# Kernel tuning notes

Measured on AMD Instinct MI355X. Metric: run time of the kernel, lower is better.

Reference implementation:

```python
import jax, jax.numpy as jnp
import numpy as np

D_MODEL = 768
N_HEADS = 12
NUM_EXPERTS = 4
TOP_K = 2
SPAN_LEN = 64
GATE_HIDDEN = 128


def setup_inputs() -> dict:
    key = jax.random.key(0)
    ks = jax.random.split(key, 14)
    B, T, C, E = 4, 4096, D_MODEL, NUM_EXPERTS
    s = 0.02
    return {
        "hidden_states": jax.random.normal(ks[0], (B, T, C), jnp.float32),
        "Wq": jax.random.normal(ks[1], (E, C, C), jnp.float32) * s,
        "bq": jnp.zeros((E, C), jnp.float32),
        "Wk": jax.random.normal(ks[2], (E, C, C), jnp.float32) * s,
        "bk": jnp.zeros((E, C), jnp.float32),
        "Wv": jax.random.normal(ks[3], (E, C, C), jnp.float32) * s,
        "bv": jnp.zeros((E, C), jnp.float32),
        "gW1": jax.random.normal(ks[4], (GATE_HIDDEN, C), jnp.float32) * s,
        "gb1": jnp.zeros((GATE_HIDDEN,), jnp.float32),
        "gW2": jax.random.normal(ks[5], (E, GATE_HIDDEN), jnp.float32) * s,
        "gb2": jnp.zeros((E,), jnp.float32),
        "Wo": jax.random.normal(ks[6], (C, C), jnp.float32) * s,
        "bo": jnp.zeros((C,), jnp.float32),
    }


def _moe_proj(w, x, W, b):
    # per-expert projection then gate-weighted sum over experts
    # x: (B,N,S,C), W: (E,O,C), w: (B,N,E)
    proj = jnp.einsum("bnsc,eoc->ebnso", x, W)          # (E,B,N,S,C)
    out = jnp.einsum("bne,ebnso->bnso", w, proj)
    out = out + jnp.einsum("bne,eo->bno", w, b)[:, :, None, :]
    return out


def reference(hidden_states, Wq, bq, Wk, bk, Wv, bv, gW1, gb1, gW2, gb2, Wo, bo):
    B, T, C = hidden_states.shape
    S, H, E, K = SPAN_LEN, N_HEADS, NUM_EXPERTS, TOP_K
    Dh = C // H
    N = T // S  # T is a multiple of span_len -> no padding, all-ones masks
    x = hidden_states.reshape(B, N, S, C)

    # gating: mean-pool per span -> MLP -> top-k softmax scattered to E slots
    pooled = x.mean(axis=2)                                  # (B,N,C)
    h = jax.nn.relu(pooled @ gW1.T + gb1)
    logits = h @ gW2.T + gb2                                 # (B,N,E)
    vals, idx = jax.lax.top_k(logits, K)
    sm = jax.nn.softmax(vals, axis=-1)                       # (B,N,K)
    w = jnp.sum(jax.nn.one_hot(idx, E, dtype=sm.dtype) * sm[..., None], axis=-2)  # (B,N,E)
    entropy = -jnp.mean(jnp.sum(w * jnp.log(jnp.clip(w, 1e-9)), axis=-1))

    # gate-weighted expert QKV projections
    q = _moe_proj(w, x, Wq, bq).reshape(B, N, S, H, Dh)
    k = _moe_proj(w, x, Wk, bk).reshape(B, N, S, H, Dh)
    v = _moe_proj(w, x, Wv, bv).reshape(B, N, S, H, Dh)

    # per-span attention (mask is all ones; dropout in eval mode)
    scores = jnp.einsum("bnshd,bnthd->bnhst", q, k) / jnp.sqrt(jnp.float32(Dh))
    attn = jax.nn.softmax(scores, axis=-1)
    out = jnp.einsum("bnhst,bnthd->bnshd", attn, v).reshape(B, T, C)
    out = out @ Wo.T + bo
    return out, entropy
```

## Files before the change

### kernel.cpp

```cpp
#include <hip/hip_runtime.h>
#include <hip/hip_bf16.h>
#include <hip/hip_fp16.h>

typedef _Float16 f16;
typedef _Float16 f16x8 __attribute__((ext_vector_type(8)));
typedef _Float16 f16x4 __attribute__((ext_vector_type(4)));
typedef float f32x4 __attribute__((ext_vector_type(4)));

constexpr int B = 4;
constexpr int T = 4096;
constexpr int C = 768;
constexpr int NH = 12;
constexpr int DH = 64;
constexpr int E = 4;
constexpr int SPAN = 64;
constexpr int N = T / SPAN;
constexpr int BN = B * N;
constexpr int GH = 128;
constexpr int BTC = B * T * C;

constexpr int U_WE = E * C * C / 8;
constexpr int U_WO = C * C / 8;
constexpr int U_WTOT = 3 * U_WE + U_WO;

__global__ __launch_bounds__(768) void cvt_x_pool(
    const float* __restrict__ x, f16* __restrict__ x16,
    float* __restrict__ pooled) {
    int span = blockIdx.x;
    int tid = threadIdx.x;
    int u = tid % 96, rg = tid / 96;
    __shared__ float part[8][C];

    const float* xb = x + (size_t)span * SPAN * C;
    f16* xo = x16 + (size_t)span * SPAN * C;
    float a8[8] = {};
    #pragma unroll
    for (int j = 0; j < 8; ++j) {
        int r = rg * 8 + j;
        const float4* s = (const float4*)(xb + (size_t)r * C + u * 8);
        float4 A = s[0], Bv = s[1];
        f16x8 o;
        o[0] = (f16)A.x;  o[1] = (f16)A.y;  o[2] = (f16)A.z;  o[3] = (f16)A.w;
        o[4] = (f16)Bv.x; o[5] = (f16)Bv.y; o[6] = (f16)Bv.z; o[7] = (f16)Bv.w;
        *(f16x8*)(xo + (size_t)r * C + u * 8) = o;
        a8[0] += A.x;  a8[1] += A.y;  a8[2] += A.z;  a8[3] += A.w;
        a8[4] += Bv.x; a8[5] += Bv.y; a8[6] += Bv.z; a8[7] += Bv.w;
    }
    #pragma unroll
    for (int j = 0; j < 8; ++j) part[rg][u * 8 + j] = a8[j];
    __syncthreads();
    float s = 0.f;
    #pragma unroll
    for (int g = 0; g < 8; ++g) s += part[g][tid];
    pooled[(size_t)span * C + tid] = s * (1.f / 64.f);
}

__global__ void cvt_w(const float* __restrict__ Wq, const float* __restrict__ Wk,
                      const float* __restrict__ Wv, const float* __restrict__ Wo,
                      f16* __restrict__ Wq16, f16* __restrict__ Wk16,
                      f16* __restrict__ Wv16, f16* __restrict__ Wo16) {
    int i = blockIdx.x * blockDim.x + threadIdx.x;
    int stride = gridDim.x * blockDim.x;
    for (; i < U_WTOT; i += stride) {
        const float* src; f16* dst; int u;
        if (i < U_WE)               { src = Wq; dst = Wq16; u = i; }
        else if (i < 2 * U_WE)      { src = Wk; dst = Wk16; u = i - U_WE; }
        else if (i < 3 * U_WE)      { src = Wv; dst = Wv16; u = i - 2 * U_WE; }
        else                        { src = Wo; dst = Wo16; u = i - 3 * U_WE; }
        float4 a = ((const float4*)src)[2 * u];
        float4 b = ((const float4*)src)[2 * u + 1];
        f16x8 o;
        o[0] = (f16)a.x; o[1] = (f16)a.y; o[2] = (f16)a.z; o[3] = (f16)a.w;
        o[4] = (f16)b.x; o[5] = (f16)b.y; o[6] = (f16)b.z; o[7] = (f16)b.w;
        ((f16x8*)dst)[u] = o;
    }
}

__global__ __launch_bounds__(128) void gate_mlp(
    const float* __restrict__ pooled,
    const float* __restrict__ gW1, const float* __restrict__ gb1,
    const float* __restrict__ gW2, const float* __restrict__ gb2,
    int* __restrict__ eidx, float* __restrict__ ewts,
    float* __restrict__ ent_partial) {
    int span = blockIdx.x;
    int tid = threadIdx.x;
    __shared__ float pl[C];
    __shared__ float h[GH];
    __shared__ float logits[E];

    for (int c = tid; c < C; c += 128) pl[c] = pooled[(size_t)span * C + c];
    __syncthreads();

    {
        float acc = gb1[tid];
        const float* wrow = gW1 + (size_t)tid * C;
        #pragma unroll 8
        for (int c = 0; c < C; ++c) acc += pl[c] * wrow[c];
        h[tid] = acc > 0.f ? acc : 0.f;
    }
    __syncthreads();

    if (tid < E) {
        float acc = gb2[tid];
        const float* wrow = gW2 + (size_t)tid * GH;
        #pragma unroll 8
        for (int j = 0; j < GH; ++j) acc += h[j] * wrow[j];
        logits[tid] = acc;
    }
    __syncthreads();

    if (tid == 0) {
        int i0 = 0; float v0 = logits[0];
        for (int e = 1; e < E; ++e) { if (logits[e] > v0) { v0 = logits[e]; i0 = e; } }
        int i1 = -1; float v1 = -3.0e38f;
        for (int e = 0; e < E; ++e) { if (e != i0 && logits[e] > v1) { v1 = logits[e]; i1 = e; } }
        float bq_ = expf(v1 - v0);
        float s = 1.f + bq_;
        float sm0 = 1.f / s;
        float sm1 = bq_ / s;
        eidx[span * 2 + 0] = i0;
        eidx[span * 2 + 1] = i1;
        ewts[span * 2 + 0] = sm0;
        ewts[span * 2 + 1] = sm1;
        float p0 = fmaxf(sm0, 1e-9f), p1 = fmaxf(sm1, 1e-9f);
        ent_partial[span] = sm0 * logf(p0) + sm1 * logf(p1);
    }
}

__global__ void entropy_kernel(const float* __restrict__ ent_partial, float* __restrict__ out_ent) {
    __shared__ float sh[256];
    int tid = threadIdx.x;
    sh[tid] = ent_partial[tid];
    __syncthreads();
    for (int s = 128; s > 0; s >>= 1) {
        if (tid < s) sh[tid] += sh[tid + s];
        __syncthreads();
    }
    if (tid == 0) *out_ent = -sh[0] * (1.0f / (float)BN);
}

__global__ __launch_bounds__(256) void qkv_mfma(
    const f16* __restrict__ xh,
    const f16* __restrict__ Wq16, const float* __restrict__ bq,
    const f16* __restrict__ Wk16, const float* __restrict__ bk,
    const f16* __restrict__ Wv16, const float* __restrict__ bv,
    const int* __restrict__ eidx, const float* __restrict__ ewts,
    f16* __restrict__ q16, f16* __restrict__ k16, f16* __restrict__ vt)
{
    int span  = blockIdx.x;
    int otile = blockIdx.y;
    int proj  = blockIdx.z;

    const f16* W; const float* bias; f16* out;
    if (proj == 0)      { W = Wq16; bias = bq; out = q16; }
    else if (proj == 1) { W = Wk16; bias = bk; out = k16; }
    else                { W = Wv16; bias = bv; out = vt; }

    int e0 = eidx[span * 2 + 0], e1 = eidx[span * 2 + 1];
    float w0 = ewts[span * 2 + 0], w1 = ewts[span * 2 + 1];
    f16 w0h = (f16)w0, w1h = (f16)w1;

    __shared__ f16x8 xs_u[64 * 8];
    __shared__ f16x8 ws_u[256 * 8];

    const f16x8* xu  = (const f16x8*)(xh + (size_t)span * 64 * C);
    const f16x8* Wu0 = (const f16x8*)(W + ((size_t)e0 * C + otile * 256) * (size_t)C);
    const f16x8* Wu1 = (const f16x8*)(W + ((size_t)e1 * C + otile * 256) * (size_t)C);

    int tid = threadIdx.x;
    int lane = tid & 63, wv = tid >> 6;
    int lr = lane & 15, lg = lane >> 4;

    f32x4 acc[4][4] = {};

    f16x8 xr[2], w0r[8], w1r[8];
    #pragma unroll
    for (int i = 0; i < 2; ++i) {
        int id = tid + i * 256;
        xr[i] = xu[(id >> 3) * 96 + (id & 7)];
    }
    #pragma unroll
    for (int i = 0; i < 8; ++i) {
        int id = tid + i * 256;
        w0r[i] = Wu0[(size_t)(id >> 3) * 96 + (id & 7)];
        w1r[i] = Wu1[(size_t)(id >> 3) * 96 + (id & 7)];
    }

    for (int kc8 = 0; kc8 < 96; kc8 += 8) {
        #pragma unroll
        for (int i = 0; i < 2; ++i) {
            int id = tid + i * 256;
            int r = id >> 3, u = id & 7;
            xs_u[r * 8 + (u ^ (r & 7))] = xr[i];
        }
        #pragma unroll
        for (int i = 0; i < 8; ++i) {
            int id = tid + i * 256;
            int r = id >> 3, u = id & 7;
            ws_u[r * 8 + (u ^ (r & 7))] = w0r[i] * w0h + w1r[i] * w1h;
        }

        if (kc8 < 88) {
            int kn = kc8 + 8;
            #pragma unroll
            for (int i = 0; i < 2; ++i) {
                int id = tid + i * 256;
                xr[i] = xu[(id >> 3) * 96 + kn + (id & 7)];
            }
            #pragma unroll
            for (int i = 0; i < 4; ++i) {
                int id = tid + i * 256;
                w0r[i] = Wu0[(size_t)(id >> 3) * 96 + kn + (id & 7)];
                w1r[i] = Wu1[(size_t)(id >> 3) * 96 + kn + (id & 7)];
            }
        }

        asm volatile("s_waitcnt lgkmcnt(0)" ::: "memory");
        __builtin_amdgcn_s_barrier();
        __builtin_amdgcn_sched_barrier(0);

        {
            int ub = lg;
            f16x8 afrag[4], bfrag[4];
            #pragma unroll
            for (int m = 0; m < 4; ++m) {
                int r = m * 16 + lr;
                afrag[m] = xs_u[r * 8 + (ub ^ (r & 7))];
            }
            #pragma unroll
            for (int n = 0; n < 4; ++n) {
                int r = wv * 64 + n * 16 + lr;
                bfrag[n] = ws_u[r * 8 + (ub ^ (r & 7))];
            }
            #pragma unroll
            for (int m = 0; m < 4; ++m)
                #pragma unroll
                for (int n = 0; n < 4; ++n)
                    acc[m][n] = __builtin_amdgcn_mfma_f32_16x16x32_f16(afrag[m], bfrag[n], acc[m][n], 0, 0, 0);
        }

        __builtin_amdgcn_sched_barrier(0);
        if (kc8 < 88) {
            int kn = kc8 + 8;
            #pragma unroll
            for (int i = 4; i < 8; ++i) {
                int id = tid + i * 256;
                w0r[i] = Wu0[(size_t)(id >> 3) * 96 + kn + (id & 7)];
                w1r[i] = Wu1[(size_t)(id >> 3) * 96 + kn + (id & 7)];
            }
        }
        __builtin_amdgcn_sched_barrier(0);

        {
            int ub = 4 + lg;
            f16x8 afrag[4], bfrag[4];
            #pragma unroll
            for (int m = 0; m < 4; ++m) {
                int r = m * 16 + lr;
                afrag[m] = xs_u[r * 8 + (ub ^ (r & 7))];
            }
            #pragma unroll
            for (int n = 0; n < 4; ++n) {
                int r = wv * 64 + n * 16 + lr;
                bfrag[n] = ws_u[r * 8 + (ub ^ (r & 7))];
            }
            #pragma unroll
            for (int m = 0; m < 4; ++m)
                #pragma unroll
                for (int n = 0; n < 4; ++n)
                    acc[m][n] = __builtin_amdgcn_mfma_f32_16x16x32_f16(afrag[m], bfrag[n], acc[m][n], 0, 0, 0);
        }

        asm volatile("s_waitcnt lgkmcnt(0)" ::: "memory");
        __builtin_amdgcn_s_barrier();
        __builtin_amdgcn_sched_barrier(0);
    }

    if (proj == 2) {
        f16* vtb = out + (size_t)span * C * 64;
        #pragma unroll
        for (int n = 0; n < 4; ++n) {
            int col = otile * 256 + wv * 64 + n * 16 + lr;
            float be = w0 * bias[(size_t)e0 * C + col] + w1 * bias[(size_t)e1 * C + col];
            #pragma unroll
            for (int m = 0; m < 4; ++m) {
                f16x4 pk;
                #pragma unroll
                for (int r = 0; r < 4; ++r) pk[r] = (f16)(acc[m][n][r] + be);
                *(f16x4*)&vtb[(size_t)col * 64 + m * 16 + lg * 4] = pk;
            }
        }
    } else {
        f16* outb = out + (size_t)span * 64 * C;
        #pragma unroll
        for (int n = 0; n < 4; ++n) {
            int col = otile * 256 + wv * 64 + n * 16 + lr;
            float be = w0 * bias[(size_t)e0 * C + col] + w1 * bias[(size_t)e1 * C + col];
            #pragma unroll
            for (int m = 0; m < 4; ++m) {
                #pragma unroll
                for (int r = 0; r < 4; ++r) {
                    int row = m * 16 + lg * 4 + r;
                    outb[(size_t)row * C + col] = (f16)(acc[m][n][r] + be);
                }
            }
        }
    }
}

__global__ __launch_bounds__(256) void attn_mfma(
    const f16* __restrict__ q16, const f16* __restrict__ k16,
    const f16* __restrict__ vt, f16* __restrict__ a16)
{
    int h = blockIdx.x, span = blockIdx.y;
    __shared__ __align__(16) f16 Klds[64 * 72];
    __shared__ __align__(16) f16 Vlds[64 * 72];
    __shared__ __align__(16) f16 Plds[64 * 72];

    int tid = threadIdx.x;
    int lane = tid & 63, mt = tid >> 6;
    int lr = lane & 15, lg = lane >> 4;

    const f16x8* ku = (const f16x8*)k16;
    const f16x8* vu = (const f16x8*)vt;
    #pragma unroll
    for (int i = 0; i < 2; ++i) {
        int id = tid + i * 256;
        int r = id >> 3, u = id & 7;
        *(f16x8*)&Klds[r * 72 + u * 8] = ku[(size_t)span * 6144 + (size_t)r * 96 + h * 8 + u];
        *(f16x8*)&Vlds[r * 72 + u * 8] = vu[(size_t)span * 6144 + (size_t)(h * 64 + r) * 8 + u];
    }
    __syncthreads();

    const f16x8* qu = (const f16x8*)q16;
    f16x8 qa[2];
    #pragma unroll
    for (int kk = 0; kk < 2; ++kk)
        qa[kk] = qu[(size_t)span * 6144 + (size_t)(mt * 16 + lr) * 96 + h * 8 + kk * 4 + lg];

    f32x4 accs[4] = {};
    #pragma unroll
    for (int nt = 0; nt < 4; ++nt) {
        #pragma unroll
        for (int kk = 0; kk < 2; ++kk) {
            f16x8 kb = *(const f16x8*)&Klds[(nt * 16 + lr) * 72 + kk * 32 + lg * 8];
            accs[nt] = __builtin_amdgcn_mfma_f32_16x16x32_f16(qa[kk], kb, accs[nt], 0, 0, 0);
        }
    }

    #pragma unroll
    for (int nt = 0; nt < 4; ++nt) accs[nt] *= 0.125f;
    f32x4 m4;
    #pragma unroll
    for (int r = 0; r < 4; ++r)
        m4[r] = fmaxf(fmaxf(accs[0][r], accs[1][r]), fmaxf(accs[2][r], accs[3][r]));
    #pragma unroll
    for (int st = 1; st < 16; st <<= 1) {
        #pragma unroll
        for (int r = 0; r < 4; ++r) m4[r] = fmaxf(m4[r], __shfl_xor(m4[r], st));
    }
    f32x4 ps[4];
    f32x4 sum4 = {0.f, 0.f, 0.f, 0.f};
    #pragma unroll
    for (int nt = 0; nt < 4; ++nt)
        #pragma unroll
        for (int r = 0; r < 4; ++r) {
            ps[nt][r] = __expf(accs[nt][r] - m4[r]);
            sum4[r] += ps[nt][r];
        }
    #pragma unroll
    for (int st = 1; st < 16; st <<= 1) {
        #pragma unroll
        for (int r = 0; r < 4; ++r) sum4[r] += __shfl_xor(sum4[r], st);
    }
    f32x4 inv4;
    #pragma unroll
    for (int r = 0; r < 4; ++r) inv4[r] = 1.0f / sum4[r];

    #pragma unroll
    for (int nt = 0; nt < 4; ++nt)
        #pragma unroll
        for (int r = 0; r < 4; ++r)
            Plds[(mt * 16 + lg * 4 + r) * 72 + nt * 16 + lr] = (f16)ps[nt][r];
    __syncthreads();

    f16x8 pa[2];
    #pragma unroll
    for (int kkt = 0; kkt < 2; ++kkt)
        pa[kkt] = *(const f16x8*)&Plds[(mt * 16 + lr) * 72 + kkt * 32 + lg * 8];
    f32x4 acco[4] = {};
    #pragma unroll
    for (int nt = 0; nt < 4; ++nt) {
        #pragma unroll
        for (int kkt = 0; kkt < 2; ++kkt) {
            f16x8 vb = *(const f16x8*)&Vlds[(nt * 16 + lr) * 72 + kkt * 32 + lg * 8];
            acco[nt] = __builtin_amdgcn_mfma_f32_16x16x32_f16(pa[kkt], vb, acco[nt], 0, 0, 0);
        }
    }

    #pragma unroll
    for (int nt = 0; nt < 4; ++nt)
        #pragma unroll
        for (int r = 0; r < 4; ++r)
            Klds[(mt * 16 + lg * 4 + r) * 72 + nt * 16 + lr] = (f16)(acco[nt][r] * inv4[r]);
    __syncthreads();

    int row = mt * 16 + (lane >> 2);
    int u2 = (lane & 3) * 2;
    f16x8 o0 = *(const f16x8*)&Klds[row * 72 + u2 * 8];
    f16x8 o1 = *(const f16x8*)&Klds[row * 72 + u2 * 8 + 8];
    f16x8* au = (f16x8*)a16;
    au[(size_t)span * 6144 + (size_t)row * 96 + h * 8 + u2]     = o0;
    au[(size_t)span * 6144 + (size_t)row * 96 + h * 8 + u2 + 1] = o1;
}

__global__ __launch_bounds__(512) void outproj_mfma(
    const f16* __restrict__ ah, const f16* __restrict__ Wo16,
    const float* __restrict__ bo, float* __restrict__ Y)
{
    int rt = blockIdx.x;
    int otile = blockIdx.y;

    __shared__ f16x8 as_u[128 * 8];
    __shared__ f16x8 ws_u[256 * 8];

    const f16x8* au  = (const f16x8*)(ah + (size_t)rt * 128 * C);
    const f16x8* Wou = (const f16x8*)(Wo16 + (size_t)otile * 256 * C);

    int tid = threadIdx.x;
    int lane = tid & 63, wv = tid >> 6;
    int lr = lane & 15, lg = lane >> 4;
    int wm = (wv >> 2) * 64;
    int wn = (wv & 3) * 64;

    f32x4 acc[4][4] = {};

    for (int kc8 = 0; kc8 < 96; kc8 += 8) {
        #pragma unroll
        for (int i = 0; i < 2; ++i) {
            int id = tid + i * 512;
            int r = id >> 3, u = id & 7;
            as_u[r * 8 + (u ^ (r & 7))] = au[(size_t)r * 96 + kc8 + u];
        }
        #pragma unroll
        for (int i = 0; i < 4; ++i) {
            int id = tid + i * 512;
            int r = id >> 3, u = id & 7;
            ws_u[r * 8 + (u ^ (r & 7))] = Wou[(size_t)r * 96 + kc8 + u];
        }
        __syncthreads();
        #pragma unroll
        for (int kk = 0; kk < 2; ++kk) {
            int ub = kk * 4 + lg;
            f16x8 afrag[4], bfrag[4];
            #pragma unroll
            for (int m = 0; m < 4; ++m) {
                int r = wm + m * 16 + lr;
                afrag[m] = as_u[r * 8 + (ub ^ (r & 7))];
            }
            #pragma unroll
            for (int n = 0; n < 4; ++n) {
                int r = wn + n * 16 + lr;
                bfrag[n] = ws_u[r * 8 + (ub ^ (r & 7))];
            }
            #pragma unroll
            for (int m = 0; m < 4; ++m)
                #pragma unroll
                for (int n = 0; n < 4; ++n)
                    acc[m][n] = __builtin_amdgcn_mfma_f32_16x16x32_f16(afrag[m], bfrag[n], acc[m][n], 0, 0, 0);
        }
        __syncthreads();
    }

    #pragma unroll
    for (int n = 0; n < 4; ++n) {
        int col = otile * 256 + wn + n * 16 + lr;
        float be = bo[col];
        #pragma unroll
        for (int m = 0; m < 4; ++m) {
            #pragma unroll
            for (int r = 0; r < 4; ++r) {
                int row = rt * 128 + wm + m * 16 + lg * 4 + r;
                Y[(size_t)row * C + col] = acc[m][n][r] + be;
            }
        }
    }
}

extern "C" void kernel_launch(void* const* d_in, const int* in_sizes, int n_in,
                              void* d_out, int out_size, void* d_ws, size_t ws_size,
                              hipStream_t stream) {
    const float* x   = (const float*)d_in[0];
    const float* Wq  = (const float*)d_in[1];
    const float* bq  = (const float*)d_in[2];
    const float* Wk  = (const float*)d_in[3];
    const float* bk  = (const float*)d_in[4];
    const float* Wv  = (const float*)d_in[5];
    const float* bv  = (const float*)d_in[6];
    const float* gW1 = (const float*)d_in[7];
    const float* gb1 = (const float*)d_in[8];
    const float* gW2 = (const float*)d_in[9];
    const float* gb2 = (const float*)d_in[10];
    const float* Wo  = (const float*)d_in[11];
    const float* bo  = (const float*)d_in[12];

    float* out = (float*)d_out;

    char* ws = (char*)d_ws;
    const size_t h_btc = (size_t)BTC * sizeof(f16);
    f16* x16  = (f16*)(ws);
    f16* q16  = (f16*)(ws + 1 * h_btc);
    f16* k16  = (f16*)(ws + 2 * h_btc);
    f16* vt16 = (f16*)(ws + 3 * h_btc);
    f16* a16  = (f16*)(ws + 4 * h_btc);
    size_t off = 5 * h_btc;
    const size_t wsz = (size_t)E * C * C * sizeof(f16);
    f16* Wq16 = (f16*)(ws + off); off += wsz;
    f16* Wk16 = (f16*)(ws + off); off += wsz;
    f16* Wv16 = (f16*)(ws + off); off += wsz;
    f16* Wo16 = (f16*)(ws + off); off += (size_t)C * C * sizeof(f16);
    int*   eidx = (int*)(ws + off); off += 2048;
    float* ewts = (float*)(ws + off); off += 2048;
    float* entp = (float*)(ws + off); off += 1024;
    float* pooled = (float*)(ws + off); off += (size_t)BN * C * sizeof(float);

    cvt_x_pool<<<dim3(BN), dim3(768), 0, stream>>>(x, x16, pooled);
    cvt_w<<<dim3(1024), dim3(256), 0, stream>>>(Wq, Wk, Wv, Wo,
                                                Wq16, Wk16, Wv16, Wo16);
    gate_mlp<<<dim3(BN), dim3(128), 0, stream>>>(pooled, gW1, gb1, gW2, gb2,
                                                 eidx, ewts, entp);
    entropy_kernel<<<dim3(1), dim3(256), 0, stream>>>(entp, out + BTC);

    qkv_mfma<<<dim3(BN, 3, 3), dim3(256), 0, stream>>>(x16, Wq16, bq, Wk16, bk, Wv16, bv,
                                                       eidx, ewts, q16, k16, vt16);
    attn_mfma<<<dim3(NH, BN), dim3(256), 0, stream>>>(q16, k16, vt16, a16);
    outproj_mfma<<<dim3(128, 3), dim3(512), 0, stream>>>(a16, Wo16, bo, out);
}
```

Measured before the change: 215.9 us.

## Shrink QKV MFMA k-chunk to 32 with padded LDS and higher occupancy

Restructures the QKV projection main loop from 64-wide k-chunks with XOR-swizzled LDS to 32-wide chunks (24 iterations) using row-padded LDS (stride 40 halfs). Fewer staging registers and the launch_bounds min-blocks hint of 3 are meant to raise occupancy. Precomputed pointers cut address arithmetic, and s_setprio brackets the MFMA burst. The cost is twice as many barriers per k and less prefetch depth per iteration, so latency hiding leans on the extra resident waves.

After: 251.3 us. +16.4%, slower.

```diff
diff --git a/kernel.cpp b/kernel.cpp
--- a/kernel.cpp
+++ b/kernel.cpp
@@ -139,7 +139,9 @@
     if (tid == 0) *out_ent = -sh[0] * (1.0f / (float)BN);
 }
 
-__global__ __launch_bounds__(256) void qkv_mfma(
+constexpr int QNCH = 24;
+
+__global__ __launch_bounds__(256, 3) void qkv_mfma(
     const f16* __restrict__ xh,
     const f16* __restrict__ Wq16, const float* __restrict__ bq,
     const f16* __restrict__ Wk16, const float* __restrict__ bk,
@@ -160,58 +162,60 @@
     float w0 = ewts[span * 2 + 0], w1 = ewts[span * 2 + 1];
     f16 w0h = (f16)w0, w1h = (f16)w1;
 
-    __shared__ f16x8 xs_u[64 * 8];
-    __shared__ f16x8 ws_u[256 * 8];
-
-    const f16x8* xu  = (const f16x8*)(xh + (size_t)span * 64 * C);
-    const f16x8* Wu0 = (const f16x8*)(W + ((size_t)e0 * C + otile * 256) * (size_t)C);
-    const f16x8* Wu1 = (const f16x8*)(W + ((size_t)e1 * C + otile * 256) * (size_t)C);
+    __shared__ __align__(16) f16 xs[64 * 40];
+    __shared__ __align__(16) f16 ws[256 * 40];
 
     int tid = threadIdx.x;
     int lane = tid & 63, wv = tid >> 6;
     int lr = lane & 15, lg = lane >> 4;
 
+    int srow = tid >> 2, su = tid & 3;
+
+    const char* xp  = (const char*)xh + ((size_t)span * 64 + srow) * 1536 + su * 16;
+    const char* w0p[4]; const char* w1p[4];
+    {
+        const char* wb0 = (const char*)W + ((size_t)e0 * C + otile * 256 + srow) * 1536 + su * 16;
+        const char* wb1 = (const char*)W + ((size_t)e1 * C + otile * 256 + srow) * 1536 + su * 16;
+        #pragma unroll
+        for (int i = 0; i < 4; ++i) {
+            w0p[i] = wb0 + (size_t)i * 64 * 1536;
+            w1p[i] = wb1 + (size_t)i * 64 * 1536;
+        }
+    }
+
+    f16* xw = &xs[srow * 40 + su * 8];
+    f16* ww = &ws[srow * 40 + su * 8];
+
+    const f16* ar[4]; const f16* br[4];
+    #pragma unroll
+    for (int m = 0; m < 4; ++m) ar[m] = &xs[(m * 16 + lr) * 40 + lg * 8];
+    #pragma unroll
+    for (int n = 0; n < 4; ++n) br[n] = &ws[(wv * 64 + n * 16 + lr) * 40 + lg * 8];
+
     f32x4 acc[4][4] = {};
 
-    f16x8 xr[2], w0r[8], w1r[8];
-    #pragma unroll
-    for (int i = 0; i < 2; ++i) {
-        int id = tid + i * 256;
-        xr[i] = xu[(id >> 3) * 96 + (id & 7)];
-    }
-    #pragma unroll
-    for (int i = 0; i < 8; ++i) {
-        int id = tid + i * 256;
-        w0r[i] = Wu0[(size_t)(id >> 3) * 96 + (id & 7)];
-        w1r[i] = Wu1[(size_t)(id >> 3) * 96 + (id & 7)];
-    }
-
-    for (int kc8 = 0; kc8 < 96; kc8 += 8) {
-        #pragma unroll
-        for (int i = 0; i < 2; ++i) {
-            int id = tid + i * 256;
-            int r = id >> 3, u = id & 7;
-            xs_u[r * 8 + (u ^ (r & 7))] = xr[i];
-        }
-        #pragma unroll
-        for (int i = 0; i < 8; ++i) {
-            int id = tid + i * 256;
-            int r = id >> 3, u = id & 7;
-            ws_u[r * 8 + (u ^ (r & 7))] = w0r[i] * w0h + w1r[i] * w1h;
-        }
-
-        if (kc8 < 88) {
-            int kn = kc8 + 8;
-            #pragma unroll
-            for (int i = 0; i < 2; ++i) {
-                int id = tid + i * 256;
-                xr[i] = xu[(id >> 3) * 96 + kn + (id & 7)];
-            }
+    f16x8 xr, w0r[4], w1r[4];
+    xr = *(const f16x8*)xp;
+    #pragma unroll
+    for (int i = 0; i < 4; ++i) {
+        w0r[i] = *(const f16x8*)w0p[i];
+        w1r[i] = *(const f16x8*)w1p[i];
+    }
+
+    for (int ch = 0; ch < QNCH; ++ch) {
+        *(f16x8*)xw = xr;
+        #pragma unroll
+        for (int i = 0; i < 4; ++i)
+            *(f16x8*)(ww + i * 2560) = w0r[i] * w0h + w1r[i] * w1h;
+
+        if (ch < QNCH - 1) {
+            xp += 64;
+            xr = *(const f16x8*)xp;
             #pragma unroll
             for (int i = 0; i < 4; ++i) {
-                int id = tid + i * 256;
-                w0r[i] = Wu0[(size_t)(id >> 3) * 96 + kn + (id & 7)];
-                w1r[i] = Wu1[(size_t)(id >> 3) * 96 + kn + (id & 7)];
+                w0p[i] += 64; w1p[i] += 64;
+                w0r[i] = *(const f16x8*)w0p[i];
+                w1r[i] = *(const f16x8*)w1p[i];
             }
         }
 
@@ -219,57 +223,18 @@
         __builtin_amdgcn_s_barrier();
         __builtin_amdgcn_sched_barrier(0);
 
-        {
-            int ub = lg;
-            f16x8 afrag[4], bfrag[4];
-            #pragma unroll
-            for (int m = 0; m < 4; ++m) {
-                int r = m * 16 + lr;
-                afrag[m] = xs_u[r * 8 + (ub ^ (r & 7))];
-            }
-            #pragma unroll
-            for (int n = 0; n < 4; ++n) {
-                int r = wv * 64 + n * 16 + lr;
-                bfrag[n] = ws_u[r * 8 + (ub ^ (r & 7))];
-            }
-            #pragma unroll
-            for (int m = 0; m < 4; ++m)
-                #pragma unroll
-                for (int n = 0; n < 4; ++n)
-                    acc[m][n] = __builtin_amdgcn_mfma_f32_16x16x32_f16(afrag[m], bfrag[n], acc[m][n], 0, 0, 0);
-        }
-
-        __builtin_amdgcn_sched_barrier(0);
-        if (kc8 < 88) {
-            int kn = kc8 + 8;
-            #pragma unroll
-            for (int i = 4; i < 8; ++i) {
-                int id = tid + i * 256;
-                w0r[i] = Wu0[(size_t)(id >> 3) * 96 + kn + (id & 7)];
-                w1r[i] = Wu1[(size_t)(id >> 3) * 96 + kn + (id & 7)];
-            }
-        }
-        __builtin_amdgcn_sched_barrier(0);
-
-        {
-            int ub = 4 + lg;
-            f16x8 afrag[4], bfrag[4];
-            #pragma unroll
-            for (int m = 0; m < 4; ++m) {
-                int r = m * 16 + lr;
-                afrag[m] = xs_u[r * 8 + (ub ^ (r & 7))];
-            }
-            #pragma unroll
-            for (int n = 0; n < 4; ++n) {
-                int r = wv * 64 + n * 16 + lr;
-                bfrag[n] = ws_u[r * 8 + (ub ^ (r & 7))];
-            }
-            #pragma unroll
-            for (int m = 0; m < 4; ++m)
-                #pragma unroll
-                for (int n = 0; n < 4; ++n)
-                    acc[m][n] = __builtin_amdgcn_mfma_f32_16x16x32_f16(afrag[m], bfrag[n], acc[m][n], 0, 0, 0);
-        }
+        f16x8 af[4], bf[4];
+        #pragma unroll
+        for (int m = 0; m < 4; ++m) af[m] = *(const f16x8*)ar[m];
+        #pragma unroll
+        for (int n = 0; n < 4; ++n) bf[n] = *(const f16x8*)br[n];
+        __builtin_amdgcn_s_setprio(1);
+        #pragma unroll
+        for (int m = 0; m < 4; ++m)
+            #pragma unroll
+            for (int n = 0; n < 4; ++n)
+                acc[m][n] = __builtin_amdgcn_mfma_f32_16x16x32_f16(af[m], bf[n], acc[m][n], 0, 0, 0);
+        __builtin_amdgcn_s_setprio(0);
 
         asm volatile("s_waitcnt lgkmcnt(0)" ::: "memory");
         __builtin_amdgcn_s_barrier();
```

## Register-prefetch out-projection tiles and use lgkm-only barriers across kernels

Applied to the files above, without the earlier changes.

The output projection now prefetches the next K-chunk of activations and Wo into registers before the LDS barrier, so global loads overlap the MFMA work. __syncthreads in the attention kernel is replaced with a barrier that waits only on LDS counters. The QKV projection no longer splits its weight prefetch across the two MFMA halves: all eight loads are issued up front and the two halves are folded into one loop. This raises register pressure and changes the interleaving of loads with MFMA issue.

After: 213.2 us. About the same (-1.3%).

```diff
diff --git a/kernel.cpp b/kernel.cpp
--- a/kernel.cpp
+++ b/kernel.cpp
@@ -22,6 +22,13 @@
 constexpr int U_WE = E * C * C / 8;
 constexpr int U_WO = C * C / 8;
 constexpr int U_WTOT = 3 * U_WE + U_WO;
+
+#define LGKM_BARRIER()                                      \
+    do {                                                    \
+        asm volatile("s_waitcnt lgkmcnt(0)" ::: "memory");  \
+        __builtin_amdgcn_s_barrier();                       \
+        __builtin_amdgcn_sched_barrier(0);                  \
+    } while (0)
 
 __global__ __launch_bounds__(768) void cvt_x_pool(
     const float* __restrict__ x, f16* __restrict__ x16,
@@ -208,19 +215,18 @@
                 xr[i] = xu[(id >> 3) * 96 + kn + (id & 7)];
             }
             #pragma unroll
-            for (int i = 0; i < 4; ++i) {
+            for (int i = 0; i < 8; ++i) {
                 int id = tid + i * 256;
                 w0r[i] = Wu0[(size_t)(id >> 3) * 96 + kn + (id & 7)];
                 w1r[i] = Wu1[(size_t)(id >> 3) * 96 + kn + (id & 7)];
             }
         }
 
-        asm volatile("s_waitcnt lgkmcnt(0)" ::: "memory");
-        __builtin_amdgcn_s_barrier();
-        __builtin_amdgcn_sched_barrier(0);
-
-        {
-            int ub = lg;
+        LGKM_BARRIER();
+
+        #pragma unroll
+        for (int kk = 0; kk < 2; ++kk) {
+            int ub = kk * 4 + lg;
             f16x8 afrag[4], bfrag[4];
             #pragma unroll
             for (int m = 0; m < 4; ++m) {
@@ -239,41 +245,7 @@
                     acc[m][n] = __builtin_amdgcn_mfma_f32_16x16x32_f16(afrag[m], bfrag[n], acc[m][n], 0, 0, 0);
         }
 
-        __builtin_amdgcn_sched_barrier(0);
-        if (kc8 < 88) {
-            int kn = kc8 + 8;
-            #pragma unroll
-            for (int i = 4; i < 8; ++i) {
-                int id = tid + i * 256;
-                w0r[i] = Wu0[(size_t)(id >> 3) * 96 + kn + (id & 7)];
-                w1r[i] = Wu1[(size_t)(id >> 3) * 96 + kn + (id & 7)];
-            }
-        }
-        __builtin_amdgcn_sched_barrier(0);
-
-        {
-            int ub = 4 + lg;
-            f16x8 afrag[4], bfrag[4];
-            #pragma unroll
-            for (int m = 0; m < 4; ++m) {
-                int r = m * 16 + lr;
-                afrag[m] = xs_u[r * 8 + (ub ^ (r & 7))];
-            }
-            #pragma unroll
-            for (int n = 0; n < 4; ++n) {
-                int r = wv * 64 + n * 16 + lr;
-                bfrag[n] = ws_u[r * 8 + (ub ^ (r & 7))];
-            }
-            #pragma unroll
-            for (int m = 0; m < 4; ++m)
-                #pragma unroll
-                for (int n = 0; n < 4; ++n)
-                    acc[m][n] = __builtin_amdgcn_mfma_f32_16x16x32_f16(afrag[m], bfrag[n], acc[m][n], 0, 0, 0);
-        }
-
-        asm volatile("s_waitcnt lgkmcnt(0)" ::: "memory");
-        __builtin_amdgcn_s_barrier();
-        __builtin_amdgcn_sched_barrier(0);
+        LGKM_BARRIER();
     }
 
     if (proj == 2) {
@@ -330,13 +302,13 @@
         *(f16x8*)&Klds[r * 72 + u * 8] = ku[(size_t)span * 6144 + (size_t)r * 96 + h * 8 + u];
         *(f16x8*)&Vlds[r * 72 + u * 8] = vu[(size_t)span * 6144 + (size_t)(h * 64 + r) * 8 + u];
     }
-    __syncthreads();
-
     const f16x8* qu = (const f16x8*)q16;
     f16x8 qa[2];
     #pragma unroll
     for (int kk = 0; kk < 2; ++kk)
         qa[kk] = qu[(size_t)span * 6144 + (size_t)(mt * 16 + lr) * 96 + h * 8 + kk * 4 + lg];
+
+    LGKM_BARRIER();
 
     f32x4 accs[4] = {};
     #pragma unroll
@@ -382,7 +354,8 @@
         #pragma unroll
         for (int r = 0; r < 4; ++r)
             Plds[(mt * 16 + lg * 4 + r) * 72 + nt * 16 + lr] = (f16)ps[nt][r];
-    __syncthreads();
+
+    LGKM_BARRIER();
 
     f16x8 pa[2];
     #pragma unroll
@@ -403,7 +376,8 @@
         #pragma unroll
         for (int r = 0; r < 4; ++r)
             Klds[(mt * 16 + lg * 4 + r) * 72 + nt * 16 + lr] = (f16)(acco[nt][r] * inv4[r]);
-    __syncthreads();
+
+    LGKM_BARRIER();
 
     int row = mt * 16 + (lane >> 2);
     int u2 = (lane & 3) * 2;
@@ -435,20 +409,48 @@
 
     f32x4 acc[4][4] = {};
 
+    f16x8 ar_[2], wr_[4];
+    #pragma unroll
+    for (int i = 0; i < 2; ++i) {
+        int id = tid + i * 512;
+        ar_[i] = au[(size_t)(id >> 3) * 96 + (id & 7)];
+    }
+    #pragma unroll
+    for (int i = 0; i < 4; ++i) {
+        int id = tid + i * 512;
+        wr_[i] = Wou[(size_t)(id >> 3) * 96 + (id & 7)];
+    }
+
     for (int kc8 = 0; kc8 < 96; kc8 += 8) {
         #pragma unroll
         for (int i = 0; i < 2; ++i) {
             int id = tid + i * 512;
             int r = id >> 3, u = id & 7;
-            as_u[r * 8 + (u ^ (r & 7))] = au[(size_t)r * 96 + kc8 + u];
+            as_u[r * 8 + (u ^ (r & 7))] = ar_[i];
         }
         #pragma unroll
         for (int i = 0; i < 4; ++i) {
             int id = tid + i * 512;
             int r = id >> 3, u = id & 7;
-            ws_u[r * 8 + (u ^ (r & 7))] = Wou[(size_t)r * 96 + kc8 + u];
-        }
-        __syncthreads();
+            ws_u[r * 8 + (u ^ (r & 7))] = wr_[i];
+        }
+
+        if (kc8 < 88) {
+            int kn = kc8 + 8;
+            #pragma unroll
+            for (int i = 0; i < 2; ++i) {
+                int id = tid + i * 512;
+                ar_[i] = au[(size_t)(id >> 3) * 96 + kn + (id & 7)];
+            }
+            #pragma unroll
+            for (int i = 0; i < 4; ++i) {
+                int id = tid + i * 512;
+                wr_[i] = Wou[(size_t)(id >> 3) * 96 + kn + (id & 7)];
+            }
+        }
+
+        LGKM_BARRIER();
+
         #pragma unroll
         for (int kk = 0; kk < 2; ++kk) {
             int ub = kk * 4 + lg;
@@ -469,7 +471,8 @@
                 for (int n = 0; n < 4; ++n)
                     acc[m][n] = __builtin_amdgcn_mfma_f32_16x16x32_f16(afrag[m], bfrag[n], acc[m][n], 0, 0, 0);
         }
-        __syncthreads();
+
+        LGKM_BARRIER();
     }
 
     #pragma unroll
```
